# Optimization experiments

Measured on AMD Instinct MI355X. Metric: run time of the kernel, lower is better.

The kernel has to match this reference:

```python
import jax, jax.numpy as jnp
import numpy as np
import math

B, C, H, W = 4, 256, 64, 64
N_GROUPS = 32
D_K = 64
N_HEADS = C // D_K  # 4
EPS = 1e-5


def setup_inputs() -> dict:
    key = jax.random.key(0)
    ks = jax.random.split(key, 7)
    return {
        "x": jax.random.normal(ks[0], (B, C, H, W), dtype=jnp.float32),
        "gamma": jax.random.uniform(ks[1], (C,), dtype=jnp.float32),
        "beta": jax.random.normal(ks[2], (C,), dtype=jnp.float32) * 0.1,
        "W_qkv": jax.random.normal(ks[3], (C, N_HEADS * D_K * 3), dtype=jnp.float32) * 0.02,
        "b_qkv": jax.random.normal(ks[4], (N_HEADS * D_K * 3,), dtype=jnp.float32) * 0.02,
        "W_out": jax.random.normal(ks[5], (N_HEADS * D_K, C), dtype=jnp.float32) * 0.02,
        "b_out": jax.random.normal(ks[6], (C,), dtype=jnp.float32) * 0.02,
    }


def _group_norm(x, gamma, beta):
    # x: [B, C, H, W], 32 groups, biased variance, eps=1e-5 (torch GroupNorm defaults)
    b, c, h, w = x.shape
    xg = x.reshape(b, N_GROUPS, c // N_GROUPS, h, w)
    mean = jnp.mean(xg, axis=(2, 3, 4), keepdims=True)
    var = jnp.var(xg, axis=(2, 3, 4), keepdims=True)
    xn = (xg - mean) / jnp.sqrt(var + EPS)
    xn = xn.reshape(b, c, h, w)
    return xn * gamma[None, :, None, None] + beta[None, :, None, None]


def reference(x, gamma, beta, W_qkv, b_qkv, W_out, b_out):
    b, c, h, w = x.shape
    n = h * w
    scale = 1.0 / math.sqrt(math.sqrt(D_K))
    # norm -> [B, N, C]
    hid = _group_norm(x, gamma, beta).reshape(b, c, n).transpose(0, 2, 1)
    # qkv projection -> [B, N, n_heads, 3*d_k], chunk on last dim
    qkv = (hid @ W_qkv + b_qkv).reshape(b, n, N_HEADS, 3 * D_K)
    q, k, v = jnp.split(qkv, 3, axis=-1)  # each [B, N, H, d_k]
    attn = jnp.einsum('bihd,bjhd->bijh', q * scale, k * scale)
    attn = jax.nn.softmax(attn, axis=2)  # softmax over j (keys)
    res = jnp.einsum('bijh,bjhd->bihd', attn, v).reshape(b, n, N_HEADS * D_K)
    res = res @ W_out + b_out  # [B, N, C]
    res = res.transpose(0, 2, 1).reshape(b, c, h, w)
    return (res + x) / math.sqrt(2.0)
```

## Files before the change

### kernel.cpp

```cpp
#include <hip/hip_runtime.h>
#include <math.h>

typedef float  f32x4  __attribute__((ext_vector_type(4)));
typedef __bf16 bf16x8 __attribute__((ext_vector_type(8)));
typedef __bf16 bf16x4 __attribute__((ext_vector_type(4)));

#define MFMA16(a, b, c) __builtin_amdgcn_mfma_f32_16x16x32_bf16((a), (b), (c), 0, 0, 0)

#define TRR(dst, a, lit)  asm volatile("ds_read_b64_tr_b16 %0, %1 offset:" lit : "=v"(dst) : "v"(a))
#define TRRM(dst, a, lit) asm volatile("ds_read_b64_tr_b16 %0, %1 offset:" lit : "=v"(dst) : "v"(a) : "memory")
#define SHUF8(a, b) __builtin_shufflevector((a), (b), 0, 1, 2, 3, 4, 5, 6, 7)

typedef __attribute__((address_space(3))) unsigned int lds_u32;
typedef __attribute__((address_space(1))) const unsigned int glb_u32;

__device__ __forceinline__ void gload16(const __bf16* g, char* l) {
    __builtin_amdgcn_global_load_lds((glb_u32*)g, (lds_u32*)l, 16, 0, 0);
}

static constexpr int BATCH = 4;
static constexpr int CH    = 256;
static constexpr int M_TOT = BATCH * 4096;

static constexpr float QSCALE = 0.18033688011112042f;

static constexpr size_t OFF_WQKV  = 0;
static constexpr size_t OFF_WOUT  = 196608ull * 2;
static constexpr size_t OFF_STATS = OFF_WOUT + 65536ull * 2;
static constexpr size_t OFF_HID   = OFF_STATS + 1024;
static constexpr size_t OFF_Q     = OFF_HID + (size_t)M_TOT * CH * 2;
static constexpr size_t OFF_K     = OFF_Q   + (size_t)M_TOT * CH * 2;
static constexpr size_t OFF_V     = OFF_K   + (size_t)M_TOT * CH * 2;

__global__ __launch_bounds__(256) void pre_kernel(const float* __restrict__ x,
                                                  float2* __restrict__ stats,
                                                  const float* __restrict__ wq,
                                                  const float* __restrict__ wo,
                                                  __bf16* __restrict__ wqf,
                                                  __bf16* __restrict__ wof) {
    if (blockIdx.x < 128) {
        int bg = blockIdx.x;
        const float4* p = (const float4*)(x + (size_t)bg * 32768);
        float s = 0.f, ss = 0.f;
        for (int i = threadIdx.x; i < 8192; i += 256) {
            float4 v = p[i];
            s  += (v.x + v.y) + (v.z + v.w);
            ss += v.x * v.x + v.y * v.y + v.z * v.z + v.w * v.w;
        }
#pragma unroll
        for (int d = 32; d > 0; d >>= 1) { s += __shfl_down(s, d); ss += __shfl_down(ss, d); }
        __shared__ float sh[8];
        int w = threadIdx.x >> 6, l = threadIdx.x & 63;
        if (l == 0) { sh[w] = s; sh[4 + w] = ss; }
        __syncthreads();
        if (threadIdx.x == 0) {
            float S = sh[0] + sh[1] + sh[2] + sh[3];
            float SS = sh[4] + sh[5] + sh[6] + sh[7];
            float mean = S * (1.f / 32768.f);
            float var  = SS * (1.f / 32768.f) - mean * mean;
            stats[bg] = make_float2(mean, rsqrtf(var + 1e-5f));
        }
    } else {
        int i = (blockIdx.x - 128) * 256 + threadIdx.x;
        if (i < 196608) {
            int e = i & 7, l = (i >> 3) & 63, kk = (i >> 9) & 7, jt = i >> 12;
            int kidx = kk * 32 + ((l >> 4) << 3) + e;
            int n = jt * 16 + (l & 15);
            wqf[i] = (__bf16)wq[kidx * 768 + n];
        } else {
            int i2 = i - 196608;
            int e = i2 & 7, l = (i2 >> 3) & 63, kk = (i2 >> 9) & 7, jt = i2 >> 12;
            int kidx = kk * 32 + ((l >> 4) << 3) + e;
            int n = jt * 16 + (l & 15);
            wof[i2] = (__bf16)wo[kidx * 256 + n];
        }
    }
}

__global__ __launch_bounds__(256) void gn_apply(const float* __restrict__ x,
                                                const float* __restrict__ gamma,
                                                const float* __restrict__ beta,
                                                const float2* __restrict__ stats,
                                                __bf16* __restrict__ hid) {
    int b  = blockIdx.x >> 6;
    int n0 = (blockIdx.x & 63) << 6;
    int c  = threadIdx.x;
    float2 st = stats[b * 32 + (c >> 3)];
    float gm = gamma[c] * st.y;
    float bt = beta[c] - st.x * gm;
    const float* xp = x + ((size_t)(b * 256 + c)) * 4096 + n0;
    __bf16* hp = hid + ((size_t)(b * 4096 + n0)) * 256 + c;
#pragma unroll
    for (int j4 = 0; j4 < 16; ++j4) {
        float4 v = *(const float4*)(xp + j4 * 4);
        hp[(size_t)(j4 * 4 + 0) * 256] = (__bf16)(v.x * gm + bt);
        hp[(size_t)(j4 * 4 + 1) * 256] = (__bf16)(v.y * gm + bt);
        hp[(size_t)(j4 * 4 + 2) * 256] = (__bf16)(v.z * gm + bt);
        hp[(size_t)(j4 * 4 + 3) * 256] = (__bf16)(v.w * gm + bt);
    }
}

__global__ __launch_bounds__(256) void qkv_gemm(const __bf16* __restrict__ hid,
                                                const __bf16* __restrict__ wf,
                                                const float* __restrict__ bqkv,
                                                __bf16* __restrict__ qb,
                                                __bf16* __restrict__ kb,
                                                __bf16* __restrict__ vb) {
    const int mt = blockIdx.x, nt = blockIdx.y;
    const int tid = threadIdx.x;
    const int w = tid >> 6, l = tid & 63;
    const int lr = l & 15, lh = l >> 4;
    f32x4 acc[4] = {{0.f,0.f,0.f,0.f},{0.f,0.f,0.f,0.f},{0.f,0.f,0.f,0.f},{0.f,0.f,0.f,0.f}};
    const __bf16* ap = hid + (size_t)(mt * 64 + w * 16 + lr) * 256 + lh * 8;
#pragma unroll
    for (int kk = 0; kk < 8; ++kk) {
        bf16x8 a = *(const bf16x8*)(ap + kk * 32);
#pragma unroll
        for (int fj = 0; fj < 4; ++fj) {
            bf16x8 bf = *(const bf16x8*)(wf + (size_t)(((nt * 4 + fj) * 8 + kk) * 64 + l) * 8);
            acc[fj] = MFMA16(a, bf, acc[fj]);
        }
    }
    int mbase = mt * 64 + w * 16 + lh * 4;
#pragma unroll
    for (int fj = 0; fj < 4; ++fj) {
        int j = nt * 64 + fj * 16 + lr;
        int head = j / 192, rem = j % 192;
        int part = rem >> 6, dd = rem & 63;
        float bias = bqkv[j];
        float sc = (part == 0) ? QSCALE : 1.0f;
        __bf16* dst = (part == 0) ? qb : (part == 1) ? kb : vb;
#pragma unroll
        for (int r = 0; r < 4; ++r) {
            int m = mbase + r;
            int b = m >> 12, n = m & 4095;
            dst[((size_t)((b * 4 + head) * 4096 + n)) * 64 + dd] = (__bf16)((acc[fj][r] + bias) * sc);
        }
    }
}

__global__ __launch_bounds__(256, 4) void attn_fwd(const __bf16* __restrict__ q,
                                                   const __bf16* __restrict__ k,
                                                   const __bf16* __restrict__ v,
                                                   __bf16* __restrict__ ao) {
    const int bh = blockIdx.y;
    const int q0 = blockIdx.x * 64;
    const int tid = threadIdx.x;
    const int wv = tid >> 6, l = tid & 63;
    const int lr = l & 15, lh = l >> 4;

    __shared__ __attribute__((aligned(16))) char smem[32768];

    const size_t base = (size_t)bh * (4096 * 64);

    const int c0 = wv * 64 + l;
    const int rK = c0 >> 3, cbK = l & 7;
    const int gk0 = rK * 64 + (cbK ^ (rK & 7)) * 8;
    const int gk1 = gk0 + 2048;
    const int dt0 = c0 >> 7, kq0 = (c0 >> 3) & 15, klo0 = (l >> 1) & 3, d80 = l & 1;
    const int gv0 = (kq0 * 4 + klo0) * 64 + dt0 * 16 + d80 * 8;
    const int gv1 = gv0 + 32;
    const int lw0 = wv * 1024;
    const int lw1 = 4096 + wv * 1024;

    const __bf16* kg = k + base;
    const __bf16* vg = v + base;

    const unsigned vAb = (unsigned)(size_t)(smem + 16384) + (unsigned)(lr * 2 + lh * 128);

    bf16x8 qf0, qf1;
    {
        const __bf16* qp = q + base + (size_t)(q0 + wv * 16 + lr) * 64 + lh * 8;
        qf0 = *(const bf16x8*)qp;
        qf1 = *(const bf16x8*)(qp + 32);
    }
    bf16x8 ones;
#pragma unroll
    for (int e = 0; e < 8; ++e) ones[e] = (__bf16)1.0f;

    f32x4 o[4] = {{0.f,0.f,0.f,0.f},{0.f,0.f,0.f,0.f},{0.f,0.f,0.f,0.f},{0.f,0.f,0.f,0.f}};
    f32x4 o4 = {0.f, 0.f, 0.f, 0.f};

    gload16(kg + gk0, smem + lw0);
    gload16(kg + gk1, smem + lw1);
    gload16(vg + gv0, smem + 16384 + lw0);
    gload16(vg + gv1, smem + 16384 + lw1);
    __syncthreads();

    unsigned voff = 0;
    for (int t = 0; t < 64; ++t) {
        if (t < 63) {
            const __bf16* kp = kg + (size_t)(t + 1) * 4096;
            const __bf16* vp = vg + (size_t)(t + 1) * 4096;
            char* kd = smem + (voff ^ 8192u);
            char* vd = smem + 16384 + (voff ^ 8192u);
            gload16(kp + gk0, kd + lw0);
            gload16(kp + gk1, kd + lw1);
            gload16(vp + gv0, vd + lw0);
            gload16(vp + gv1, vd + lw1);
        }

        const char* Kc = smem + voff;
        f32x4 s[4];
        const f32x4 z = {0.f, 0.f, 0.f, 0.f};
        __builtin_amdgcn_s_setprio(1);
#pragma unroll
        for (int fj = 0; fj < 4; ++fj) {
            int row = fj * 16 + lr;
            bf16x8 kb0 = *(const bf16x8*)(Kc + row * 128 + ((lh * 16) ^ ((row & 7) << 4)));
            bf16x8 kb1 = *(const bf16x8*)(Kc + row * 128 + (((4 + lh) * 16) ^ ((row & 7) << 4)));
            s[fj] = MFMA16(kb0, qf0, z);
            s[fj] = MFMA16(kb1, qf1, s[fj]);
        }
        __builtin_amdgcn_s_setprio(0);

        bf16x8 B0, B1;
#pragma unroll
        for (int fj = 0; fj < 4; ++fj)
#pragma unroll
            for (int r = 0; r < 4; ++r) {
                float p = __builtin_amdgcn_exp2f(s[fj][r]);
                if (fj < 2) B0[fj * 4 + r] = (__bf16)p;
                else        B1[(fj - 2) * 4 + r] = (__bf16)p;
            }

        unsigned vA = vAb + voff;
        bf16x4 t0, t1, t2, t3, t4, t5, t6, t7;
        TRRM(t0, vA, "0");    TRR(t1, vA, "512");
        TRR(t2, vA, "1024");  TRR(t3, vA, "1536");
        TRR(t4, vA, "2048");  TRR(t5, vA, "2560");
        TRR(t6, vA, "3072");  TRR(t7, vA, "3584");
        asm volatile("s_waitcnt lgkmcnt(0)" ::: "memory");
        __builtin_amdgcn_sched_barrier(0);
        __builtin_amdgcn_s_setprio(1);
        o4   = MFMA16(ones, B0, o4);
        o[0] = MFMA16(SHUF8(t0, t1), B0, o[0]);
        o[0] = MFMA16(SHUF8(t2, t3), B1, o[0]);
        o[1] = MFMA16(SHUF8(t4, t5), B0, o[1]);
        o[1] = MFMA16(SHUF8(t6, t7), B1, o[1]);
        __builtin_amdgcn_s_setprio(0);
        TRR(t0, vA, "4096");  TRR(t1, vA, "4608");
        TRR(t2, vA, "5120");  TRR(t3, vA, "5632");
        TRR(t4, vA, "6144");  TRR(t5, vA, "6656");
        TRR(t6, vA, "7168");  TRR(t7, vA, "7680");
        asm volatile("s_waitcnt lgkmcnt(0)" ::: "memory");
        __builtin_amdgcn_sched_barrier(0);
        __builtin_amdgcn_s_setprio(1);
        o4   = MFMA16(ones, B1, o4);
        o[2] = MFMA16(SHUF8(t0, t1), B0, o[2]);
        o[2] = MFMA16(SHUF8(t2, t3), B1, o[2]);
        o[3] = MFMA16(SHUF8(t4, t5), B0, o[3]);
        o[3] = MFMA16(SHUF8(t6, t7), B1, o[3]);
        __builtin_amdgcn_s_setprio(0);

        __syncthreads();
        voff ^= 8192u;
    }

    float inv = 1.0f / o4[0];
    int b = bh >> 2, h = bh & 3;
    int n = q0 + wv * 16 + lr;
    __bf16* dst = ao + ((size_t)(b * 4096 + n)) * 256 + h * 64 + lh * 4;
#pragma unroll
    for (int fd = 0; fd < 4; ++fd) {
        bf16x4 pk;
#pragma unroll
        for (int r = 0; r < 4; ++r) pk[r] = (__bf16)(o[fd][r] * inv);
        *(bf16x4*)(dst + fd * 16) = pk;
    }
}

__global__ __launch_bounds__(256) void out_gemm(const __bf16* __restrict__ ao,
                                                const __bf16* __restrict__ wf,
                                                const float* __restrict__ bout,
                                                const float* __restrict__ x,
                                                float* __restrict__ out) {
    const int mt = blockIdx.x, nt = blockIdx.y;
    const int tid = threadIdx.x;
    const int w = tid >> 6, l = tid & 63;
    const int lr = l & 15, lh = l >> 4;
    f32x4 acc[4] = {{0.f,0.f,0.f,0.f},{0.f,0.f,0.f,0.f},{0.f,0.f,0.f,0.f},{0.f,0.f,0.f,0.f}};
    const __bf16* ap = ao + (size_t)(mt * 64 + w * 16 + lr) * 256 + lh * 8;
#pragma unroll
    for (int kk = 0; kk < 8; ++kk) {
        bf16x8 a = *(const bf16x8*)(ap + kk * 32);
#pragma unroll
        for (int fj = 0; fj < 4; ++fj) {
            bf16x8 bf = *(const bf16x8*)(wf + (size_t)(((nt * 4 + fj) * 8 + kk) * 64 + l) * 8);
            acc[fj] = MFMA16(a, bf, acc[fj]);
        }
    }
    __shared__ float tile[64][72];
#pragma unroll
    for (int fj = 0; fj < 4; ++fj) {
        float bias = bout[nt * 64 + fj * 16 + lr];
#pragma unroll
        for (int r = 0; r < 4; ++r)
            tile[w * 16 + lh * 4 + r][fj * 16 + lr] = acc[fj][r] + bias;
    }
    __syncthreads();
    int b  = mt >> 6;
    int n0 = (mt & 63) * 64;
    int c0 = nt * 64;
    int cl = tid >> 2, nq = tid & 3;
    size_t gbase = ((size_t)(b * 256 + c0 + cl)) * 4096 + n0 + nq * 16;
#pragma unroll
    for (int i = 0; i < 16; i += 4) {
        float4 xv = *(const float4*)(x + gbase + i);
        float4 ov;
        ov.x = (tile[nq * 16 + i + 0][cl] + xv.x) * 0.70710678118654752f;
        ov.y = (tile[nq * 16 + i + 1][cl] + xv.y) * 0.70710678118654752f;
        ov.z = (tile[nq * 16 + i + 2][cl] + xv.z) * 0.70710678118654752f;
        ov.w = (tile[nq * 16 + i + 3][cl] + xv.w) * 0.70710678118654752f;
        *(float4*)(out + gbase + i) = ov;
    }
}

extern "C" void kernel_launch(void* const* d_in, const int* in_sizes, int n_in,
                              void* d_out, int out_size, void* d_ws, size_t ws_size,
                              hipStream_t stream) {
    const float* x     = (const float*)d_in[0];
    const float* gamma = (const float*)d_in[1];
    const float* beta  = (const float*)d_in[2];
    const float* W_qkv = (const float*)d_in[3];
    const float* b_qkv = (const float*)d_in[4];
    const float* W_out = (const float*)d_in[5];
    const float* b_out = (const float*)d_in[6];
    float* out = (float*)d_out;
    char* ws = (char*)d_ws;

    __bf16* wqf   = (__bf16*)(ws + OFF_WQKV);
    __bf16* wof   = (__bf16*)(ws + OFF_WOUT);
    float2* stats = (float2*)(ws + OFF_STATS);
    __bf16* hid   = (__bf16*)(ws + OFF_HID);
    __bf16* qb    = (__bf16*)(ws + OFF_Q);
    __bf16* kb    = (__bf16*)(ws + OFF_K);
    __bf16* vb    = (__bf16*)(ws + OFF_V);

    pre_kernel<<<1152, 256, 0, stream>>>(x, stats, W_qkv, W_out, wqf, wof);
    gn_apply<<<256, 256, 0, stream>>>(x, gamma, beta, stats, hid);
    qkv_gemm<<<dim3(256, 12), 256, 0, stream>>>(hid, wqf, b_qkv, qb, kb, vb);
    attn_fwd<<<dim3(64, 16), 256, 0, stream>>>(qb, kb, vb, hid);
    out_gemm<<<dim3(256, 4), 256, 0, stream>>>(hid, wof, b_out, x, out);
}
```

Baseline: 146.7 us.

## Fuse group-norm apply into QKV GEMM via LDS and unroll attention loop by two

The separate gn_apply kernel is removed. Each QKV block now normalizes its 64-token tile of x into a swizzled LDS buffer and computes all 16 column tiles for one of q/k/v, so the bf16 hid tensor no longer makes a round trip through global memory and one launch disappears. The grid shrinks from 256x12 to 256x3 blocks, each holding 16 accumulators, which raises register pressure and cuts parallelism. Each block also redoes the normalization of its tile three times, once per q/k/v block. The attention loop is manually unrolled by two with constant LDS buffer offsets, replacing the runtime voff xor.

```diff
diff --git a/kernel.cpp b/kernel.cpp
--- a/kernel.cpp
+++ b/kernel.cpp
@@ -77,64 +77,72 @@
     }
 }
 
-__global__ __launch_bounds__(256) void gn_apply(const float* __restrict__ x,
-                                                const float* __restrict__ gamma,
-                                                const float* __restrict__ beta,
-                                                const float2* __restrict__ stats,
-                                                __bf16* __restrict__ hid) {
-    int b  = blockIdx.x >> 6;
-    int n0 = (blockIdx.x & 63) << 6;
-    int c  = threadIdx.x;
-    float2 st = stats[b * 32 + (c >> 3)];
-    float gm = gamma[c] * st.y;
-    float bt = beta[c] - st.x * gm;
-    const float* xp = x + ((size_t)(b * 256 + c)) * 4096 + n0;
-    __bf16* hp = hid + ((size_t)(b * 4096 + n0)) * 256 + c;
-#pragma unroll
-    for (int j4 = 0; j4 < 16; ++j4) {
-        float4 v = *(const float4*)(xp + j4 * 4);
-        hp[(size_t)(j4 * 4 + 0) * 256] = (__bf16)(v.x * gm + bt);
-        hp[(size_t)(j4 * 4 + 1) * 256] = (__bf16)(v.y * gm + bt);
-        hp[(size_t)(j4 * 4 + 2) * 256] = (__bf16)(v.z * gm + bt);
-        hp[(size_t)(j4 * 4 + 3) * 256] = (__bf16)(v.w * gm + bt);
-    }
-}
-
-__global__ __launch_bounds__(256) void qkv_gemm(const __bf16* __restrict__ hid,
-                                                const __bf16* __restrict__ wf,
-                                                const float* __restrict__ bqkv,
-                                                __bf16* __restrict__ qb,
-                                                __bf16* __restrict__ kb,
-                                                __bf16* __restrict__ vb) {
-    const int mt = blockIdx.x, nt = blockIdx.y;
+__global__ __launch_bounds__(256) void qkv_gn(const float* __restrict__ x,
+                                              const float* __restrict__ gamma,
+                                              const float* __restrict__ beta,
+                                              const float2* __restrict__ stats,
+                                              const __bf16* __restrict__ wf,
+                                              const float* __restrict__ bqkv,
+                                              __bf16* __restrict__ qb,
+                                              __bf16* __restrict__ kb,
+                                              __bf16* __restrict__ vb) {
+    const int mt = blockIdx.x;
+    const int p  = blockIdx.y;
     const int tid = threadIdx.x;
+    const int b  = mt >> 6;
+    const int n0 = (mt & 63) * 64;
+
+    __shared__ __attribute__((aligned(16))) char At[64 * 512];
+
+    {
+        const int c = tid;
+        float2 st = stats[b * 32 + (c >> 3)];
+        float gm = gamma[c] * st.y;
+        float bt = beta[c] - st.x * gm;
+        const float* xp = x + ((size_t)(b * 256 + c)) * 4096 + n0;
+        const unsigned cx = (unsigned)(c * 2);
+#pragma unroll
+        for (int j4 = 0; j4 < 16; ++j4) {
+            float4 vv = *(const float4*)(xp + j4 * 4);
+            float pv[4] = {vv.x, vv.y, vv.z, vv.w};
+#pragma unroll
+            for (int i = 0; i < 4; ++i) {
+                int tk = j4 * 4 + i;
+                *(__bf16*)(At + tk * 512 + (cx ^ ((tk & 7) << 4))) = (__bf16)(pv[i] * gm + bt);
+            }
+        }
+    }
+    __syncthreads();
+
     const int w = tid >> 6, l = tid & 63;
     const int lr = l & 15, lh = l >> 4;
-    f32x4 acc[4] = {{0.f,0.f,0.f,0.f},{0.f,0.f,0.f,0.f},{0.f,0.f,0.f,0.f},{0.f,0.f,0.f,0.f}};
-    const __bf16* ap = hid + (size_t)(mt * 64 + w * 16 + lr) * 256 + lh * 8;
+    const int tk = w * 16 + lr;
+    f32x4 acc[16];
+#pragma unroll
+    for (int fj = 0; fj < 16; ++fj) acc[fj] = (f32x4){0.f, 0.f, 0.f, 0.f};
+
 #pragma unroll
     for (int kk = 0; kk < 8; ++kk) {
-        bf16x8 a = *(const bf16x8*)(ap + kk * 32);
-#pragma unroll
-        for (int fj = 0; fj < 4; ++fj) {
-            bf16x8 bf = *(const bf16x8*)(wf + (size_t)(((nt * 4 + fj) * 8 + kk) * 64 + l) * 8);
-            acc[fj] = MFMA16(a, bf, acc[fj]);
-        }
-    }
-    int mbase = mt * 64 + w * 16 + lh * 4;
-#pragma unroll
-    for (int fj = 0; fj < 4; ++fj) {
-        int j = nt * 64 + fj * 16 + lr;
-        int head = j / 192, rem = j % 192;
-        int part = rem >> 6, dd = rem & 63;
-        float bias = bqkv[j];
-        float sc = (part == 0) ? QSCALE : 1.0f;
-        __bf16* dst = (part == 0) ? qb : (part == 1) ? kb : vb;
+        bf16x8 a = *(const bf16x8*)(At + tk * 512 + ((kk * 64 + lh * 16) ^ ((tk & 7) << 4)));
+#pragma unroll
+        for (int fj = 0; fj < 16; ++fj) {
+            int jt = (fj >> 2) * 12 + p * 4 + (fj & 3);
+            bf16x8 bfr = *(const bf16x8*)(wf + (size_t)(((jt * 8 + kk) * 64 + l) * 8));
+            acc[fj] = MFMA16(a, bfr, acc[fj]);
+        }
+    }
+
+    __bf16* dst = (p == 0) ? qb : (p == 1) ? kb : vb;
+    const float sc = (p == 0) ? QSCALE : 1.0f;
+#pragma unroll
+    for (int fj = 0; fj < 16; ++fj) {
+        int h = fj >> 2;
+        int dd = (fj & 3) * 16 + lr;
+        float bias = bqkv[h * 192 + p * 64 + dd];
 #pragma unroll
         for (int r = 0; r < 4; ++r) {
-            int m = mbase + r;
-            int b = m >> 12, n = m & 4095;
-            dst[((size_t)((b * 4 + head) * 4096 + n)) * 64 + dd] = (__bf16)((acc[fj][r] + bias) * sc);
+            int n = n0 + w * 16 + lh * 4 + r;
+            dst[((size_t)((b * 4 + h) * 4096 + n)) * 64 + dd] = (__bf16)((acc[fj][r] + bias) * sc);
         }
     }
 }
@@ -166,7 +174,8 @@
     const __bf16* kg = k + base;
     const __bf16* vg = v + base;
 
-    const unsigned vAb = (unsigned)(size_t)(smem + 16384) + (unsigned)(lr * 2 + lh * 128);
+    const unsigned vA0 = (unsigned)(size_t)(smem + 16384) + (unsigned)(lr * 2 + lh * 128);
+    const unsigned vA1 = vA0 + 8192u;
 
     bf16x8 qf0, qf1;
     {
@@ -187,20 +196,16 @@
     gload16(vg + gv1, smem + 16384 + lw1);
     __syncthreads();
 
-    unsigned voff = 0;
-    for (int t = 0; t < 64; ++t) {
-        if (t < 63) {
-            const __bf16* kp = kg + (size_t)(t + 1) * 4096;
-            const __bf16* vp = vg + (size_t)(t + 1) * 4096;
-            char* kd = smem + (voff ^ 8192u);
-            char* vd = smem + 16384 + (voff ^ 8192u);
+    auto body = [&](const char* Kc, unsigned vA, char* kd, char* vd, int tnext) {
+        if (tnext < 64) {
+            const __bf16* kp = kg + (size_t)tnext * 4096;
+            const __bf16* vp = vg + (size_t)tnext * 4096;
             gload16(kp + gk0, kd + lw0);
             gload16(kp + gk1, kd + lw1);
             gload16(vp + gv0, vd + lw0);
             gload16(vp + gv1, vd + lw1);
         }
 
-        const char* Kc = smem + voff;
         f32x4 s[4];
         const f32x4 z = {0.f, 0.f, 0.f, 0.f};
         __builtin_amdgcn_s_setprio(1);
@@ -219,12 +224,11 @@
         for (int fj = 0; fj < 4; ++fj)
 #pragma unroll
             for (int r = 0; r < 4; ++r) {
-                float p = __builtin_amdgcn_exp2f(s[fj][r]);
-                if (fj < 2) B0[fj * 4 + r] = (__bf16)p;
-                else        B1[(fj - 2) * 4 + r] = (__bf16)p;
+                float pp = __builtin_amdgcn_exp2f(s[fj][r]);
+                if (fj < 2) B0[fj * 4 + r] = (__bf16)pp;
+                else        B1[(fj - 2) * 4 + r] = (__bf16)pp;
             }
 
-        unsigned vA = vAb + voff;
         bf16x4 t0, t1, t2, t3, t4, t5, t6, t7;
         TRRM(t0, vA, "0");    TRR(t1, vA, "512");
         TRR(t2, vA, "1024");  TRR(t3, vA, "1536");
@@ -254,7 +258,11 @@
         __builtin_amdgcn_s_setprio(0);
 
         __syncthreads();
-        voff ^= 8192u;
+    };
+
+    for (int t = 0; t < 64; t += 2) {
+        body(smem,        vA0, smem + 8192, smem + 16384 + 8192, t + 1);
+        body(smem + 8192, vA1, smem,        smem + 16384,        t + 2);
     }
 
     float inv = 1.0f / o4[0];
@@ -338,8 +346,7 @@
     __bf16* vb    = (__bf16*)(ws + OFF_V);
 
     pre_kernel<<<1152, 256, 0, stream>>>(x, stats, W_qkv, W_out, wqf, wof);
-    gn_apply<<<256, 256, 0, stream>>>(x, gamma, beta, stats, hid);
-    qkv_gemm<<<dim3(256, 12), 256, 0, stream>>>(hid, wqf, b_qkv, qb, kb, vb);
+    qkv_gn<<<dim3(256, 3), 256, 0, stream>>>(x, gamma, beta, stats, wqf, b_qkv, qb, kb, vb);
     attn_fwd<<<dim3(64, 16), 256, 0, stream>>>(qb, kb, vb, hid);
     out_gemm<<<dim3(256, 4), 256, 0, stream>>>(hid, wof, b_out, x, out);
 }
```

Result: slower. 153.3 us (+4.5%).

## Use 16x16x16 MFMA for PV with direct transposed operands, unroll double buffer, remap blocks

Applied to the files above, without the earlier changes.

The PV product in attention now uses v_mfma_f32_16x16x16_bf16 via inline asm. This lets each transposed LDS read feed an MFMA directly instead of concatenating pairs with shuffles, and the V global-to-LDS layout is permuted to match. The main loop is unrolled by two so buffer offsets are compile-time constants, and a 1D grid with a swizzled block-to-(head,query tile) mapping replaces the 2D grid to change L2 locality. This trades twice as many smaller MFMAs and hand-placed s_nop hazard padding for fewer register moves and address arithmetic.

```diff
diff --git a/kernel.cpp b/kernel.cpp
--- a/kernel.cpp
+++ b/kernel.cpp
@@ -6,10 +6,11 @@
 typedef __bf16 bf16x4 __attribute__((ext_vector_type(4)));
 
 #define MFMA16(a, b, c) __builtin_amdgcn_mfma_f32_16x16x32_bf16((a), (b), (c), 0, 0, 0)
+#define MFMA16A(acc, a, b) \
+    asm volatile("v_mfma_f32_16x16x16_bf16 %0, %1, %2, %0" : "+v"(acc) : "v"(a), "v"(b))
 
 #define TRR(dst, a, lit)  asm volatile("ds_read_b64_tr_b16 %0, %1 offset:" lit : "=v"(dst) : "v"(a))
 #define TRRM(dst, a, lit) asm volatile("ds_read_b64_tr_b16 %0, %1 offset:" lit : "=v"(dst) : "v"(a) : "memory")
-#define SHUF8(a, b) __builtin_shufflevector((a), (b), 0, 1, 2, 3, 4, 5, 6, 7)
 
 typedef __attribute__((address_space(3))) unsigned int lds_u32;
 typedef __attribute__((address_space(1))) const unsigned int glb_u32;
@@ -143,8 +144,10 @@
                                                    const __bf16* __restrict__ k,
                                                    const __bf16* __restrict__ v,
                                                    __bf16* __restrict__ ao) {
-    const int bh = blockIdx.y;
-    const int q0 = blockIdx.x * 64;
+    const int id = blockIdx.x;
+    const int within = id >> 3;
+    const int bh = ((id & 7) << 1) + (within >> 6);
+    const int q0 = (within & 63) * 64;
     const int tid = threadIdx.x;
     const int wv = tid >> 6, l = tid & 63;
     const int lr = l & 15, lh = l >> 4;
@@ -157,16 +160,19 @@
     const int rK = c0 >> 3, cbK = l & 7;
     const int gk0 = rK * 64 + (cbK ^ (rK & 7)) * 8;
     const int gk1 = gk0 + 2048;
-    const int dt0 = c0 >> 7, kq0 = (c0 >> 3) & 15, klo0 = (l >> 1) & 3, d80 = l & 1;
-    const int gv0 = (kq0 * 4 + klo0) * 64 + dt0 * 16 + d80 * 8;
-    const int gv1 = gv0 + 32;
+    auto vsrc = [](int c) -> int {
+        int ks = c >> 7, fd = (c >> 5) & 3, g = (c >> 3) & 3, j = (c >> 1) & 3, d8 = c & 1;
+        return (ks * 16 + g * 4 + j) * 64 + fd * 16 + d8 * 8;
+    };
+    const int gv0 = vsrc(c0), gv1 = vsrc(c0 + 256);
     const int lw0 = wv * 1024;
     const int lw1 = 4096 + wv * 1024;
 
     const __bf16* kg = k + base;
     const __bf16* vg = v + base;
 
-    const unsigned vAb = (unsigned)(size_t)(smem + 16384) + (unsigned)(lr * 2 + lh * 128);
+    const unsigned vA0 = (unsigned)(size_t)(smem + 16384) + (unsigned)(lr * 2 + lh * 128);
+    const unsigned vA1 = vA0 + 8192u;
 
     bf16x8 qf0, qf1;
     {
@@ -174,9 +180,9 @@
         qf0 = *(const bf16x8*)qp;
         qf1 = *(const bf16x8*)(qp + 32);
     }
-    bf16x8 ones;
-#pragma unroll
-    for (int e = 0; e < 8; ++e) ones[e] = (__bf16)1.0f;
+    bf16x4 ones4;
+#pragma unroll
+    for (int e = 0; e < 4; ++e) ones4[e] = (__bf16)1.0f;
 
     f32x4 o[4] = {{0.f,0.f,0.f,0.f},{0.f,0.f,0.f,0.f},{0.f,0.f,0.f,0.f},{0.f,0.f,0.f,0.f}};
     f32x4 o4 = {0.f, 0.f, 0.f, 0.f};
@@ -187,20 +193,16 @@
     gload16(vg + gv1, smem + 16384 + lw1);
     __syncthreads();
 
-    unsigned voff = 0;
-    for (int t = 0; t < 64; ++t) {
-        if (t < 63) {
-            const __bf16* kp = kg + (size_t)(t + 1) * 4096;
-            const __bf16* vp = vg + (size_t)(t + 1) * 4096;
-            char* kd = smem + (voff ^ 8192u);
-            char* vd = smem + 16384 + (voff ^ 8192u);
+    auto body = [&](const char* Kc, unsigned vA, char* kd, char* vd, int tnext) {
+        if (tnext < 64) {
+            const __bf16* kp = kg + (size_t)tnext * 4096;
+            const __bf16* vp = vg + (size_t)tnext * 4096;
             gload16(kp + gk0, kd + lw0);
             gload16(kp + gk1, kd + lw1);
             gload16(vp + gv0, vd + lw0);
             gload16(vp + gv1, vd + lw1);
         }
 
-        const char* Kc = smem + voff;
         f32x4 s[4];
         const f32x4 z = {0.f, 0.f, 0.f, 0.f};
         __builtin_amdgcn_s_setprio(1);
@@ -214,17 +216,15 @@
         }
         __builtin_amdgcn_s_setprio(0);
 
-        bf16x8 B0, B1;
-#pragma unroll
-        for (int fj = 0; fj < 4; ++fj)
-#pragma unroll
-            for (int r = 0; r < 4; ++r) {
-                float p = __builtin_amdgcn_exp2f(s[fj][r]);
-                if (fj < 2) B0[fj * 4 + r] = (__bf16)p;
-                else        B1[(fj - 2) * 4 + r] = (__bf16)p;
-            }
-
-        unsigned vA = vAb + voff;
+        bf16x4 Bv0, Bv1, Bv2, Bv3;
+#pragma unroll
+        for (int r = 0; r < 4; ++r) {
+            Bv0[r] = (__bf16)__builtin_amdgcn_exp2f(s[0][r]);
+            Bv1[r] = (__bf16)__builtin_amdgcn_exp2f(s[1][r]);
+            Bv2[r] = (__bf16)__builtin_amdgcn_exp2f(s[2][r]);
+            Bv3[r] = (__bf16)__builtin_amdgcn_exp2f(s[3][r]);
+        }
+
         bf16x4 t0, t1, t2, t3, t4, t5, t6, t7;
         TRRM(t0, vA, "0");    TRR(t1, vA, "512");
         TRR(t2, vA, "1024");  TRR(t3, vA, "1536");
@@ -233,11 +233,16 @@
         asm volatile("s_waitcnt lgkmcnt(0)" ::: "memory");
         __builtin_amdgcn_sched_barrier(0);
         __builtin_amdgcn_s_setprio(1);
-        o4   = MFMA16(ones, B0, o4);
-        o[0] = MFMA16(SHUF8(t0, t1), B0, o[0]);
-        o[0] = MFMA16(SHUF8(t2, t3), B1, o[0]);
-        o[1] = MFMA16(SHUF8(t4, t5), B0, o[1]);
-        o[1] = MFMA16(SHUF8(t6, t7), B1, o[1]);
+        MFMA16A(o4,   ones4, Bv0);
+        MFMA16A(o[0], t0, Bv0);
+        MFMA16A(o[1], t1, Bv0);
+        MFMA16A(o[2], t2, Bv0);
+        MFMA16A(o[3], t3, Bv0);
+        MFMA16A(o4,   ones4, Bv1);
+        MFMA16A(o[0], t4, Bv1);
+        MFMA16A(o[1], t5, Bv1);
+        MFMA16A(o[2], t6, Bv1);
+        MFMA16A(o[3], t7, Bv1);
         __builtin_amdgcn_s_setprio(0);
         TRR(t0, vA, "4096");  TRR(t1, vA, "4608");
         TRR(t2, vA, "5120");  TRR(t3, vA, "5632");
@@ -246,16 +251,27 @@
         asm volatile("s_waitcnt lgkmcnt(0)" ::: "memory");
         __builtin_amdgcn_sched_barrier(0);
         __builtin_amdgcn_s_setprio(1);
-        o4   = MFMA16(ones, B1, o4);
-        o[2] = MFMA16(SHUF8(t0, t1), B0, o[2]);
-        o[2] = MFMA16(SHUF8(t2, t3), B1, o[2]);
-        o[3] = MFMA16(SHUF8(t4, t5), B0, o[3]);
-        o[3] = MFMA16(SHUF8(t6, t7), B1, o[3]);
+        MFMA16A(o4,   ones4, Bv2);
+        MFMA16A(o[0], t0, Bv2);
+        MFMA16A(o[1], t1, Bv2);
+        MFMA16A(o[2], t2, Bv2);
+        MFMA16A(o[3], t3, Bv2);
+        MFMA16A(o4,   ones4, Bv3);
+        MFMA16A(o[0], t4, Bv3);
+        MFMA16A(o[1], t5, Bv3);
+        MFMA16A(o[2], t6, Bv3);
+        MFMA16A(o[3], t7, Bv3);
         __builtin_amdgcn_s_setprio(0);
 
         __syncthreads();
-        voff ^= 8192u;
-    }
+    };
+
+    for (int t = 0; t < 64; t += 2) {
+        body(smem,        vA0, smem + 8192, smem + 16384 + 8192, t + 1);
+        body(smem + 8192, vA1, smem,        smem + 16384,        t + 2);
+    }
+
+    asm volatile("s_nop 7\n\ts_nop 7");
 
     float inv = 1.0f / o4[0];
     int b = bh >> 2, h = bh & 3;
@@ -340,6 +356,6 @@
     pre_kernel<<<1152, 256, 0, stream>>>(x, stats, W_qkv, W_out, wqf, wof);
     gn_apply<<<256, 256, 0, stream>>>(x, gamma, beta, stats, hid);
     qkv_gemm<<<dim3(256, 12), 256, 0, stream>>>(hid, wqf, b_qkv, qb, kb, vb);
-    attn_fwd<<<dim3(64, 16), 256, 0, stream>>>(qb, kb, vb, hid);
+    attn_fwd<<<1024, 256, 0, stream>>>(qb, kb, vb, hid);
     out_gemm<<<dim3(256, 4), 256, 0, stream>>>(hid, wof, b_out, x, out);
 }
```

Result: slower. 155.7 us (+6.1%).

## Remap attention blocks for XCD-local K/V reuse and unroll double-buffered loop

Applied to the files above, without the earlier changes.

Switches attention to a 1D grid and remaps block ids so that consecutive blocks, which round-robin across the XCDs, cover two batch-heads per XCD. Sharing K/V this way should improve L2 reuse. The main loop is unrolled by two with fixed LDS buffer addresses, which removes the runtime voff XOR. All 16 transposed V reads are now issued before the exp2 softmax, behind a single wait instead of two, so LDS latency can overlap with the exponentials. In exchange, register pressure rises from holding 16 V fragments at once, which could hurt occupancy at the 4-block launch bound.

```diff
diff --git a/kernel.cpp b/kernel.cpp
--- a/kernel.cpp
+++ b/kernel.cpp
@@ -143,8 +143,10 @@
                                                    const __bf16* __restrict__ k,
                                                    const __bf16* __restrict__ v,
                                                    __bf16* __restrict__ ao) {
-    const int bh = blockIdx.y;
-    const int q0 = blockIdx.x * 64;
+    const int id = blockIdx.x;
+    const int within = id >> 3;
+    const int bh = ((id & 7) << 1) + (within >> 6);
+    const int q0 = (within & 63) * 64;
     const int tid = threadIdx.x;
     const int wv = tid >> 6, l = tid & 63;
     const int lr = l & 15, lh = l >> 4;
@@ -166,7 +168,8 @@
     const __bf16* kg = k + base;
     const __bf16* vg = v + base;
 
-    const unsigned vAb = (unsigned)(size_t)(smem + 16384) + (unsigned)(lr * 2 + lh * 128);
+    const unsigned vA0 = (unsigned)(size_t)(smem + 16384) + (unsigned)(lr * 2 + lh * 128);
+    const unsigned vA1 = vA0 + 8192u;
 
     bf16x8 qf0, qf1;
     {
@@ -187,20 +190,16 @@
     gload16(vg + gv1, smem + 16384 + lw1);
     __syncthreads();
 
-    unsigned voff = 0;
-    for (int t = 0; t < 64; ++t) {
-        if (t < 63) {
-            const __bf16* kp = kg + (size_t)(t + 1) * 4096;
-            const __bf16* vp = vg + (size_t)(t + 1) * 4096;
-            char* kd = smem + (voff ^ 8192u);
-            char* vd = smem + 16384 + (voff ^ 8192u);
+    auto body = [&](const char* Kc, unsigned vA, char* kd, char* vd, int tnext) {
+        if (tnext < 64) {
+            const __bf16* kp = kg + (size_t)tnext * 4096;
+            const __bf16* vp = vg + (size_t)tnext * 4096;
             gload16(kp + gk0, kd + lw0);
             gload16(kp + gk1, kd + lw1);
             gload16(vp + gv0, vd + lw0);
             gload16(vp + gv1, vd + lw1);
         }
 
-        const char* Kc = smem + voff;
         f32x4 s[4];
         const f32x4 z = {0.f, 0.f, 0.f, 0.f};
         __builtin_amdgcn_s_setprio(1);
@@ -214,47 +213,47 @@
         }
         __builtin_amdgcn_s_setprio(0);
 
+        bf16x4 u0, u1, u2, u3, u4, u5, u6, u7, u8, u9, u10, u11, u12, u13, u14, u15;
+        TRRM(u0,  vA, "0");    TRR(u1,  vA, "512");
+        TRR(u2,  vA, "1024");  TRR(u3,  vA, "1536");
+        TRR(u4,  vA, "2048");  TRR(u5,  vA, "2560");
+        TRR(u6,  vA, "3072");  TRR(u7,  vA, "3584");
+        TRR(u8,  vA, "4096");  TRR(u9,  vA, "4608");
+        TRR(u10, vA, "5120");  TRR(u11, vA, "5632");
+        TRR(u12, vA, "6144");  TRR(u13, vA, "6656");
+        TRR(u14, vA, "7168");  TRR(u15, vA, "7680");
+
         bf16x8 B0, B1;
 #pragma unroll
         for (int fj = 0; fj < 4; ++fj)
 #pragma unroll
             for (int r = 0; r < 4; ++r) {
-                float p = __builtin_amdgcn_exp2f(s[fj][r]);
-                if (fj < 2) B0[fj * 4 + r] = (__bf16)p;
-                else        B1[(fj - 2) * 4 + r] = (__bf16)p;
+                float pp = __builtin_amdgcn_exp2f(s[fj][r]);
+                if (fj < 2) B0[fj * 4 + r] = (__bf16)pp;
+                else        B1[(fj - 2) * 4 + r] = (__bf16)pp;
             }
 
-        unsigned vA = vAb + voff;
-        bf16x4 t0, t1, t2, t3, t4, t5, t6, t7;
-        TRRM(t0, vA, "0");    TRR(t1, vA, "512");
-        TRR(t2, vA, "1024");  TRR(t3, vA, "1536");
-        TRR(t4, vA, "2048");  TRR(t5, vA, "2560");
-        TRR(t6, vA, "3072");  TRR(t7, vA, "3584");
         asm volatile("s_waitcnt lgkmcnt(0)" ::: "memory");
         __builtin_amdgcn_sched_barrier(0);
         __builtin_amdgcn_s_setprio(1);
         o4   = MFMA16(ones, B0, o4);
-        o[0] = MFMA16(SHUF8(t0, t1), B0, o[0]);
-        o[0] = MFMA16(SHUF8(t2, t3), B1, o[0]);
-        o[1] = MFMA16(SHUF8(t4, t5), B0, o[1]);
-        o[1] = MFMA16(SHUF8(t6, t7), B1, o[1]);
+        o[0] = MFMA16(SHUF8(u0,  u1),  B0, o[0]);
+        o[0] = MFMA16(SHUF8(u2,  u3),  B1, o[0]);
+        o[1] = MFMA16(SHUF8(u4,  u5),  B0, o[1]);
+        o[1] = MFMA16(SHUF8(u6,  u7),  B1, o[1]);
+        o4   = MFMA16(ones, B1, o4);
+        o[2] = MFMA16(SHUF8(u8,  u9),  B0, o[2]);
+        o[2] = MFMA16(SHUF8(u10, u11), B1, o[2]);
+        o[3] = MFMA16(SHUF8(u12, u13), B0, o[3]);
+        o[3] = MFMA16(SHUF8(u14, u15), B1, o[3]);
         __builtin_amdgcn_s_setprio(0);
-        TRR(t0, vA, "4096");  TRR(t1, vA, "4608");
-        TRR(t2, vA, "5120");  TRR(t3, vA, "5632");
-        TRR(t4, vA, "6144");  TRR(t5, vA, "6656");
-        TRR(t6, vA, "7168");  TRR(t7, vA, "7680");
-        asm volatile("s_waitcnt lgkmcnt(0)" ::: "memory");
-        __builtin_amdgcn_sched_barrier(0);
-        __builtin_amdgcn_s_setprio(1);
-        o4   = MFMA16(ones, B1, o4);
-        o[2] = MFMA16(SHUF8(t0, t1), B0, o[2]);
-        o[2] = MFMA16(SHUF8(t2, t3), B1, o[2]);
-        o[3] = MFMA16(SHUF8(t4, t5), B0, o[3]);
-        o[3] = MFMA16(SHUF8(t6, t7), B1, o[3]);
-        __builtin_amdgcn_s_setprio(0);
 
         __syncthreads();
-        voff ^= 8192u;
+    };
+
+    for (int t = 0; t < 64; t += 2) {
+        body(smem,        vA0, smem + 8192, smem + 16384 + 8192, t + 1);
+        body(smem + 8192, vA1, smem,        smem + 16384,        t + 2);
     }
 
     float inv = 1.0f / o4[0];
@@ -340,6 +339,6 @@
     pre_kernel<<<1152, 256, 0, stream>>>(x, stats, W_qkv, W_out, wqf, wof);
     gn_apply<<<256, 256, 0, stream>>>(x, gamma, beta, stats, hid);
     qkv_gemm<<<dim3(256, 12), 256, 0, stream>>>(hid, wqf, b_qkv, qb, kb, vb);
-    attn_fwd<<<dim3(64, 16), 256, 0, stream>>>(qb, kb, vb, hid);
+    attn_fwd<<<1024, 256, 0, stream>>>(qb, kb, vb, hid);
     out_gemm<<<dim3(256, 4), 256, 0, stream>>>(hid, wof, b_out, x, out);
 }
```

Measured after the change: 144.4 us. About the same (-1.6%).
